# Performance work log

Hardware: AMD Instinct MI355X
Metric: run time of the kernel (lower is better)

Reference implementation:

```python
import jax, jax.numpy as jnp
import numpy as np

B1, B2, D = 8192, 12288, 128


def setup_inputs() -> dict:
    key = jax.random.key(0)
    k1, k2 = jax.random.split(key)
    desc1 = jax.random.normal(k1, (B1, D), dtype=jnp.float32)
    desc2 = jax.random.normal(k2, (B2, D), dtype=jnp.float32)
    return {"desc1": desc1, "desc2": desc2}


def reference(desc1, desc2):
    # Pairwise L2 distance (torch.cdist, p=2) via the expanded form to avoid
    sq1 = jnp.sum(desc1 * desc1, axis=1, keepdims=True)          # (B1, 1)
    sq2 = jnp.sum(desc2 * desc2, axis=1)                          # (B2,)
    cost = jnp.sqrt(jnp.maximum(sq1 + sq2 - 2.0 * (desc1 @ desc2.T), 0.0))  # (B1, B2)

    b1, b2 = cost.shape
    ms = min(b1, b2)

    match_dists = jnp.min(cost, axis=1)    # (B1,) row minima
    idxs_in_2 = jnp.argmin(cost, axis=1)   # (B1,)
    match_dists2 = jnp.min(cost, axis=0)   # (B2,) col minima
    idxs_in_1 = jnp.argmin(cost, axis=0)   # (B2,)

    minsize_idxs = jnp.arange(ms)
    if b1 <= b2:  # static shape comparison -> Python if is fine
        mutual_nns = minsize_idxs == idxs_in_1[idxs_in_2][:ms]
        dists = match_dists[:ms]
        matches_idxs = jnp.stack([minsize_idxs, idxs_in_2[:ms]], axis=1)
    else:
        mutual_nns = minsize_idxs == idxs_in_2[idxs_in_1][:ms]
        dists = match_dists2[:ms]
        matches_idxs = jnp.stack([idxs_in_1[:ms], minsize_idxs], axis=1)

    # jit-compatible fixed-size output: non-mutual rows are masked with
    # dist=+inf and idx=-1 instead of boolean-compressed as in torch.
    match_dists_out = jnp.where(mutual_nns, dists, jnp.inf).reshape(-1, 1)  # (ms, 1)
    matches_idxs_out = jnp.where(mutual_nns[:, None], matches_idxs, -1)      # (ms, 2)
    return match_dists_out, matches_idxs_out, mutual_nns
```

## Files before the change

### kernel.cpp

```cpp
#include <hip/hip_runtime.h>
#include <math.h>

#define NB1 8192
#define NB2 12288
#define DD  128

typedef unsigned long long u64;
typedef unsigned short ushort_t;
typedef __attribute__((ext_vector_type(8))) short short8;
typedef __attribute__((ext_vector_type(4))) float f32x4;

__device__ __forceinline__ float bigf() { return __uint_as_float(0x7F7F0000u); }

__device__ __forceinline__ unsigned orderbits(float v) {
    unsigned b = __float_as_uint(v);
    return b ^ ((unsigned)((int)b >> 31) | 0x80000000u);
}
__device__ __forceinline__ float unorderbits(unsigned k) {
    unsigned b = (k & 0x80000000u) ? (k ^ 0x80000000u) : ~k;
    return __uint_as_float(b);
}
__device__ __forceinline__ u64 packkey(float v, unsigned idx) {
    return ((u64)orderbits(v) << 32) | idx;
}
__device__ __forceinline__ u64 umin64(u64 a, u64 b) { return a < b ? a : b; }

__device__ __forceinline__ ushort_t bf_rn(float x) {
    unsigned u = __float_as_uint(x);
    return (ushort_t)((u + 0x7FFFu + ((u >> 16) & 1u)) >> 16);
}
__device__ __forceinline__ float bf_up(ushort_t h) {
    return __uint_as_float(((unsigned)h) << 16);
}
__device__ __forceinline__ int fswz(int r) { return (r + (r >> 2)) & 3; }

__global__ __launch_bounds__(256) void prep_kernel(
    const float* __restrict__ d1, const float* __restrict__ d2,
    float* __restrict__ sq1, float* __restrict__ sq2,
    u64* __restrict__ rowmin, u64* __restrict__ colmin) {
    int t = blockIdx.x * 256 + threadIdx.x;
    if (t < NB1) {
        rowmin[t] = ~0ull;
        const float4* p = (const float4*)(d1 + (size_t)t * DD);
        float s = 0.f;
        #pragma unroll
        for (int c = 0; c < DD / 4; ++c) {
            float4 v = p[c];
            s = fmaf(v.x, v.x, s); s = fmaf(v.y, v.y, s);
            s = fmaf(v.z, v.z, s); s = fmaf(v.w, v.w, s);
        }
        sq1[t] = s;
    }
    if (t < NB2) {
        colmin[t] = ~0ull;
        const float4* p = (const float4*)(d2 + (size_t)t * DD);
        float s = 0.f;
        #pragma unroll
        for (int c = 0; c < DD / 4; ++c) {
            float4 v = p[c];
            s = fmaf(v.x, v.x, s); s = fmaf(v.y, v.y, s);
            s = fmaf(v.z, v.z, s); s = fmaf(v.w, v.w, s);
        }
        sq2[t] = s;
    }
}

__global__ __launch_bounds__(256) void split_frag_kernel(
    const float* __restrict__ d1, const float* __restrict__ d2,
    ushort_t* __restrict__ Af, ushort_t* __restrict__ Bf) {
    int t = blockIdx.x * 256 + threadIdx.x;
    int lane = t & 63;
    int task = t >> 6;
    bool isA = task < 2048;
    int lt = isA ? task : task - 2048;
    int rb = lt >> 2;
    int kc = lt & 3;
    int row = rb * 16 + (lane & 15);
    int kst = kc * 32 + (lane >> 4) * 8;
    const float* src = (isA ? d1 : d2) + (size_t)row * DD + kst;
    size_t pstride = (size_t)(isA ? NB1 : NB2) * DD;
    ushort_t* dst = (isA ? Af : Bf) + ((size_t)lt * 512 + lane * 8);

    short8 H, M, L;
    #pragma unroll
    for (int e = 0; e < 8; ++e) {
        float x = src[e];
        ushort_t h = bf_rn(x); float r1 = x - bf_up(h);
        ushort_t m = bf_rn(r1); float r2 = r1 - bf_up(m);
        H[e] = (short)h; M[e] = (short)m; L[e] = (short)bf_rn(r2);
    }
    *(short8*)(dst)                = H;
    *(short8*)(dst + pstride)      = M;
    *(short8*)(dst + 2 * pstride)  = L;
}

__global__ __launch_bounds__(256) void mfma_tile3_kernel(
    const ushort_t* __restrict__ Af, const ushort_t* __restrict__ Bf,
    const float* __restrict__ sq1, const float* __restrict__ sq2,
    u64* __restrict__ rowmin, u64* __restrict__ colmin)
{
    const int bid  = blockIdx.x;
    const int xcd  = bid & 7;
    const int t_   = bid >> 3;
    const int kch  = t_ >> 6;
    const int wdn  = t_ & 63;
    const int cj   = wdn & 7;
    const int ci   = wdn >> 3;
    const int j0b  = (kch * 8 + cj) * 128;
    const int i0b  = (xcd * 8 + ci) * 128;

    const int tid  = threadIdx.x;
    const int lane = tid & 63;
    const int wid  = tid >> 6;
    const int wr   = wid >> 1;
    const int wc   = wid & 1;
    const int lrow = lane & 15;
    const int lg   = lane >> 4;

    const ushort_t* abase = Af + ((size_t)((i0b >> 4) + wr * 4) * 2048) + lane * 8;
    const ushort_t* bbase = Bf + ((size_t)((j0b >> 4) + wc * 4) * 2048) + lane * 8;
    const size_t apl = (size_t)512 * 2048;
    const size_t bpl = (size_t)768 * 2048;

    f32x4 acc[4][4];
    #pragma unroll
    for (int mi = 0; mi < 4; ++mi)
        #pragma unroll
        for (int ni = 0; ni < 4; ++ni)
            acc[mi][ni] = (f32x4){0.f, 0.f, 0.f, 0.f};

    #pragma unroll 1
    for (int kc = 0; kc < 4; ++kc) {
        const int ko = kc * 512;
        short8 bfr[3][4];
        #pragma unroll
        for (int c = 0; c < 3; ++c)
            #pragma unroll
            for (int ni = 0; ni < 4; ++ni)
                bfr[c][ni] = *(const short8*)(bbase + c * bpl + ni * 2048 + ko);
        short8 a0[3], a1[3];
        #pragma unroll
        for (int c = 0; c < 3; ++c)
            a0[c] = *(const short8*)(abase + c * apl + ko);
        #pragma unroll
        for (int mi = 0; mi < 4; ++mi) {
            if (mi < 3) {
                #pragma unroll
                for (int c = 0; c < 3; ++c)
                    a1[c] = *(const short8*)(abase + c * apl + (mi + 1) * 2048 + ko);
            }
            #pragma unroll
            for (int ni = 0; ni < 4; ++ni) {
                f32x4 a = acc[mi][ni];
                a = __builtin_amdgcn_mfma_f32_16x16x32_bf16(a0[0], bfr[0][ni], a, 0, 0, 0);
                a = __builtin_amdgcn_mfma_f32_16x16x32_bf16(a0[0], bfr[1][ni], a, 0, 0, 0);
                a = __builtin_amdgcn_mfma_f32_16x16x32_bf16(a0[1], bfr[0][ni], a, 0, 0, 0);
                a = __builtin_amdgcn_mfma_f32_16x16x32_bf16(a0[0], bfr[2][ni], a, 0, 0, 0);
                a = __builtin_amdgcn_mfma_f32_16x16x32_bf16(a0[1], bfr[1][ni], a, 0, 0, 0);
                a = __builtin_amdgcn_mfma_f32_16x16x32_bf16(a0[2], bfr[0][ni], a, 0, 0, 0);
                acc[mi][ni] = a;
            }
            #pragma unroll
            for (int c = 0; c < 3; ++c) a0[c] = a1[c];
        }
    }

    float q2v[4];
    #pragma unroll
    for (int ni = 0; ni < 4; ++ni)
        q2v[ni] = sq2[j0b + wc * 64 + ni * 16 + lrow];
    float4 q1v[4];
    #pragma unroll
    for (int mi = 0; mi < 4; ++mi)
        q1v[mi] = *(const float4*)(sq1 + i0b + wr * 64 + mi * 16 + 4 * lg);

    #pragma unroll
    for (int mi = 0; mi < 4; ++mi)
        #pragma unroll
        for (int r = 0; r < 4; ++r) {
            u64 best = ~0ull;
            #pragma unroll
            for (int ni = 0; ni < 4; ++ni) {
                float kr = fmaf(-2.f, acc[mi][ni][r], q2v[ni]);
                best = umin64(best, packkey(kr, (unsigned)(j0b + wc * 64 + ni * 16 + lrow)));
            }
            #pragma unroll
            for (int mask = 8; mask; mask >>= 1)
                best = umin64(best, __shfl_xor(best, mask));
            if (lrow == 0)
                atomicMin(&rowmin[i0b + wr * 64 + mi * 16 + 4 * lg + r], best);
        }

    #pragma unroll
    for (int ni = 0; ni < 4; ++ni) {
        u64 best = ~0ull;
        #pragma unroll
        for (int mi = 0; mi < 4; ++mi) {
            const float* q1p = (const float*)&q1v[mi];
            #pragma unroll
            for (int r = 0; r < 4; ++r) {
                float kc_ = fmaf(-2.f, acc[mi][ni][r], q1p[r]);
                best = umin64(best, packkey(kc_, (unsigned)(i0b + wr * 64 + mi * 16 + 4 * lg + r)));
            }
        }
        best = umin64(best, __shfl_xor(best, 16));
        best = umin64(best, __shfl_xor(best, 32));
        if (lane < 16)
            atomicMin(&colmin[j0b + wc * 64 + ni * 16 + lrow], best);
    }
}

__global__ __launch_bounds__(256) void mfma_tile_kernel(
    const float* __restrict__ d1, const float* __restrict__ d2,
    const float* __restrict__ sq1, const float* __restrict__ sq2,
    u64* __restrict__ rowmin, u64* __restrict__ colmin)
{
    __shared__ __align__(16) short lds[6 * 4096];
    const int tid = threadIdx.x;
    const int i0b = blockIdx.y * 128;
    const int j0b = blockIdx.x * 128;
    const int srow  = tid >> 1;
    const int shalf = tid & 1;
    const int sfr   = fswz(srow);
    const int sg0   = ((2 * shalf) ^ sfr) * 8;
    const int sg1   = ((2 * shalf + 1) ^ sfr) * 8;
    const float* gA = d1 + (size_t)(i0b + srow) * DD + shalf * 16;
    const float* gB = d2 + (size_t)(j0b + srow) * DD + shalf * 16;
    short* wA = lds + srow * 32;
    short* wB = lds + 3 * 4096 + srow * 32;
    const int lane = tid & 63;
    const int wid  = tid >> 6;
    const int wr   = wid >> 1;
    const int wc   = wid & 1;
    const int lrow = lane & 15;
    const int lg   = lane >> 4;
    const int gx   = (lg ^ fswz(lrow)) * 8;
    const int aoff = (wr * 64 + lrow) * 32 + gx;
    const int boff = 3 * 4096 + (wc * 64 + lrow) * 32 + gx;

    f32x4 acc[4][4];
    #pragma unroll
    for (int mi = 0; mi < 4; ++mi)
        #pragma unroll
        for (int ni = 0; ni < 4; ++ni)
            acc[mi][ni] = (f32x4){0.f, 0.f, 0.f, 0.f};

    for (int kc = 0; kc < 4; ++kc) {
        {
            const float* sp = gA + kc * 32;
            short8 H0, M0, L0, H1, M1, L1;
            #pragma unroll
            for (int e = 0; e < 8; ++e) {
                float x = sp[e];
                ushort_t h = bf_rn(x); float r1 = x - bf_up(h);
                ushort_t m = bf_rn(r1); float r2 = r1 - bf_up(m);
                H0[e] = (short)h; M0[e] = (short)m; L0[e] = (short)bf_rn(r2);
            }
            #pragma unroll
            for (int e = 0; e < 8; ++e) {
                float x = sp[8 + e];
                ushort_t h = bf_rn(x); float r1 = x - bf_up(h);
                ushort_t m = bf_rn(r1); float r2 = r1 - bf_up(m);
                H1[e] = (short)h; M1[e] = (short)m; L1[e] = (short)bf_rn(r2);
            }
            *(short8*)(wA + sg0)        = H0;
            *(short8*)(wA + sg1)        = H1;
            *(short8*)(wA + 4096 + sg0) = M0;
            *(short8*)(wA + 4096 + sg1) = M1;
            *(short8*)(wA + 8192 + sg0) = L0;
            *(short8*)(wA + 8192 + sg1) = L1;
        }
        {
            const float* sp = gB + kc * 32;
            short8 H0, M0, L0, H1, M1, L1;
            #pragma unroll
            for (int e = 0; e < 8; ++e) {
                float x = sp[e];
                ushort_t h = bf_rn(x); float r1 = x - bf_up(h);
                ushort_t m = bf_rn(r1); float r2 = r1 - bf_up(m);
                H0[e] = (short)h; M0[e] = (short)m; L0[e] = (short)bf_rn(r2);
            }
            #pragma unroll
            for (int e = 0; e < 8; ++e) {
                float x = sp[8 + e];
                ushort_t h = bf_rn(x); float r1 = x - bf_up(h);
                ushort_t m = bf_rn(r1); float r2 = r1 - bf_up(m);
                H1[e] = (short)h; M1[e] = (short)m; L1[e] = (short)bf_rn(r2);
            }
            *(short8*)(wB + sg0)        = H0;
            *(short8*)(wB + sg1)        = H1;
            *(short8*)(wB + 4096 + sg0) = M0;
            *(short8*)(wB + 4096 + sg1) = M1;
            *(short8*)(wB + 8192 + sg0) = L0;
            *(short8*)(wB + 8192 + sg1) = L1;
        }
        __syncthreads();
        short8 af[3][4], bfr[3][4];
        #pragma unroll
        for (int c = 0; c < 3; ++c)
            #pragma unroll
            for (int t = 0; t < 4; ++t) {
                af[c][t]  = *(const short8*)(lds + c * 4096 + aoff + t * 512);
                bfr[c][t] = *(const short8*)(lds + c * 4096 + boff + t * 512);
            }
        #pragma unroll
        for (int mi = 0; mi < 4; ++mi)
            #pragma unroll
            for (int ni = 0; ni < 4; ++ni) {
                f32x4 a = acc[mi][ni];
                a = __builtin_amdgcn_mfma_f32_16x16x32_bf16(af[0][mi], bfr[0][ni], a, 0, 0, 0);
                a = __builtin_amdgcn_mfma_f32_16x16x32_bf16(af[0][mi], bfr[1][ni], a, 0, 0, 0);
                a = __builtin_amdgcn_mfma_f32_16x16x32_bf16(af[1][mi], bfr[0][ni], a, 0, 0, 0);
                a = __builtin_amdgcn_mfma_f32_16x16x32_bf16(af[0][mi], bfr[2][ni], a, 0, 0, 0);
                a = __builtin_amdgcn_mfma_f32_16x16x32_bf16(af[1][mi], bfr[1][ni], a, 0, 0, 0);
                a = __builtin_amdgcn_mfma_f32_16x16x32_bf16(af[2][mi], bfr[0][ni], a, 0, 0, 0);
                acc[mi][ni] = a;
            }
        __syncthreads();
    }

    float q2v[4];
    #pragma unroll
    for (int ni = 0; ni < 4; ++ni)
        q2v[ni] = sq2[j0b + wc * 64 + ni * 16 + lrow];
    float4 q1v[4];
    #pragma unroll
    for (int mi = 0; mi < 4; ++mi)
        q1v[mi] = *(const float4*)(sq1 + i0b + wr * 64 + mi * 16 + 4 * lg);

    #pragma unroll
    for (int mi = 0; mi < 4; ++mi)
        #pragma unroll
        for (int r = 0; r < 4; ++r) {
            u64 best = ~0ull;
            #pragma unroll
            for (int ni = 0; ni < 4; ++ni) {
                float kr = fmaf(-2.f, acc[mi][ni][r], q2v[ni]);
                best = umin64(best, packkey(kr, (unsigned)(j0b + wc * 64 + ni * 16 + lrow)));
            }
            #pragma unroll
            for (int mask = 8; mask; mask >>= 1)
                best = umin64(best, __shfl_xor(best, mask));
            if (lrow == 0)
                atomicMin(&rowmin[i0b + wr * 64 + mi * 16 + 4 * lg + r], best);
        }
    #pragma unroll
    for (int ni = 0; ni < 4; ++ni) {
        u64 best = ~0ull;
        #pragma unroll
        for (int mi = 0; mi < 4; ++mi) {
            const float* q1p = (const float*)&q1v[mi];
            #pragma unroll
            for (int r = 0; r < 4; ++r) {
                float kc_ = fmaf(-2.f, acc[mi][ni][r], q1p[r]);
                best = umin64(best, packkey(kc_, (unsigned)(i0b + wr * 64 + mi * 16 + 4 * lg + r)));
            }
        }
        best = umin64(best, __shfl_xor(best, 16));
        best = umin64(best, __shfl_xor(best, 32));
        if (lane < 16)
            atomicMin(&colmin[j0b + wc * 64 + ni * 16 + lrow], best);
    }
}

__global__ __launch_bounds__(256) void final_kernel(
    const float* __restrict__ sq1,
    const u64* __restrict__ rowmin, const u64* __restrict__ colmin,
    float* __restrict__ out) {
    int i = blockIdx.x * 256 + threadIdx.x;
    if (i >= NB1) return;
    u64 rm = rowmin[i];
    unsigned ju = (unsigned)(rm & 0xFFFFFFFFu);
    float kr = unorderbits((unsigned)(rm >> 32));
    float dist = sqrtf(fmaxf(sq1[i] + kr, 0.f));
    dist = fminf(dist, bigf());
    bool valid = (ju < (unsigned)NB2);
    int j = valid ? (int)ju : 0;
    u64 cm = colmin[j];
    int i2 = (int)(cm & 0xFFFFFFFFu);
    bool mut = valid && (i2 == i);
    out[i] = mut ? dist : bigf();
    out[NB1 + 2 * i]     = mut ? (float)i : -1.f;
    out[NB1 + 2 * i + 1] = mut ? (float)j : -1.f;
    out[NB1 + 2 * NB1 + i] = mut ? 1.f : 0.f;
}

extern "C" void kernel_launch(void* const* d_in, const int* in_sizes, int n_in,
                              void* d_out, int out_size, void* d_ws, size_t ws_size,
                              hipStream_t stream) {
    const float* d1 = (const float*)d_in[0];
    const float* d2 = (const float*)d_in[1];
    float* out = (float*)d_out;

    char* ws = (char*)d_ws;
    float* sq1    = (float*)(ws);
    float* sq2    = (float*)(ws + 32768);
    u64*   rowmin = (u64*)(ws + 81920);
    u64*   colmin = (u64*)(ws + 147456);
    ushort_t* Af = (ushort_t*)(ws + 245760);
    ushort_t* Bf = (ushort_t*)(ws + 245760 + 6291456);
    const size_t need = 245760 + 6291456 + 9437184;

    hipLaunchKernelGGL(prep_kernel, dim3((NB2 + 255) / 256), dim3(256), 0, stream,
                       d1, d2, sq1, sq2, rowmin, colmin);
    if (ws_size >= need) {
        hipLaunchKernelGGL(split_frag_kernel, dim3(1280), dim3(256), 0, stream,
                           d1, d2, Af, Bf);
        hipLaunchKernelGGL(mfma_tile3_kernel, dim3((NB2 / 128) * (NB1 / 128)), dim3(256), 0, stream,
                           Af, Bf, sq1, sq2, rowmin, colmin);
    } else {
        hipLaunchKernelGGL(mfma_tile_kernel, dim3(NB2 / 128, NB1 / 128), dim3(256), 0, stream,
                           d1, d2, sq1, sq2, rowmin, colmin);
    }
    hipLaunchKernelGGL(final_kernel, dim3((NB1 + 255) / 256), dim3(256), 0, stream,
                       sq1, rowmin, colmin, out);
}
```

Baseline: 192.8 us.

## Interleave bf16 split planes per fragment and double-buffer B loads across k-chunks

The split kernel now stores the high, mid and low bf16 planes next to each other for each fragment, instead of in three separate plane arrays far apart. The GEMM kernel reads them with small contiguous offsets. The k-chunk loop is fully unrolled, with B fragments double-buffered and the next chunk's A fragment prefetched, so global loads overlap the MFMA work. This is meant to hide load latency and improve locality, at the cost of more live registers, which may reduce occupancy or cause spills.

After: 195.2 us. About the same (+1.3%).

```diff
diff --git a/kernel.cpp b/kernel.cpp
--- a/kernel.cpp
+++ b/kernel.cpp
@@ -33,6 +33,7 @@
     return __uint_as_float(((unsigned)h) << 16);
 }
 __device__ __forceinline__ int fswz(int r) { return (r + (r >> 2)) & 3; }
+__device__ __forceinline__ short8 ld8(const ushort_t* p) { return *(const short8*)p; }
 
 __global__ __launch_bounds__(256) void prep_kernel(
     const float* __restrict__ d1, const float* __restrict__ d2,
@@ -78,8 +79,7 @@
     int row = rb * 16 + (lane & 15);
     int kst = kc * 32 + (lane >> 4) * 8;
     const float* src = (isA ? d1 : d2) + (size_t)row * DD + kst;
-    size_t pstride = (size_t)(isA ? NB1 : NB2) * DD;
-    ushort_t* dst = (isA ? Af : Bf) + ((size_t)lt * 512 + lane * 8);
+    ushort_t* dst = (isA ? Af : Bf) + ((size_t)lt * 1536 + lane * 8);
 
     short8 H, M, L;
     #pragma unroll
@@ -89,9 +89,9 @@
         ushort_t m = bf_rn(r1); float r2 = r1 - bf_up(m);
         H[e] = (short)h; M[e] = (short)m; L[e] = (short)bf_rn(r2);
     }
-    *(short8*)(dst)                = H;
-    *(short8*)(dst + pstride)      = M;
-    *(short8*)(dst + 2 * pstride)  = L;
+    *(short8*)(dst)        = H;
+    *(short8*)(dst + 512)  = M;
+    *(short8*)(dst + 1024) = L;
 }
 
 __global__ __launch_bounds__(256) void mfma_tile3_kernel(
@@ -117,10 +117,8 @@
     const int lrow = lane & 15;
     const int lg   = lane >> 4;
 
-    const ushort_t* abase = Af + ((size_t)((i0b >> 4) + wr * 4) * 2048) + lane * 8;
-    const ushort_t* bbase = Bf + ((size_t)((j0b >> 4) + wc * 4) * 2048) + lane * 8;
-    const size_t apl = (size_t)512 * 2048;
-    const size_t bpl = (size_t)768 * 2048;
+    const ushort_t* abase = Af + ((size_t)((i0b >> 4) + wr * 4) * 6144) + lane * 8;
+    const ushort_t* bbase = Bf + ((size_t)((j0b >> 4) + wc * 4) * 6144) + lane * 8;
 
     f32x4 acc[4][4];
     #pragma unroll
@@ -129,35 +127,47 @@
         for (int ni = 0; ni < 4; ++ni)
             acc[mi][ni] = (f32x4){0.f, 0.f, 0.f, 0.f};
 
-    #pragma unroll 1
+    short8 bufA[3][4], bufB[3][4];
+    short8 a0[3], a1[3];
+    #pragma unroll
+    for (int c = 0; c < 3; ++c) {
+        #pragma unroll
+        for (int ni = 0; ni < 4; ++ni)
+            bufA[c][ni] = ld8(bbase + ni * 6144 + c * 512);
+        a0[c] = ld8(abase + c * 512);
+    }
+
+    #pragma unroll
     for (int kc = 0; kc < 4; ++kc) {
-        const int ko = kc * 512;
-        short8 bfr[3][4];
-        #pragma unroll
-        for (int c = 0; c < 3; ++c)
-            #pragma unroll
-            for (int ni = 0; ni < 4; ++ni)
-                bfr[c][ni] = *(const short8*)(bbase + c * bpl + ni * 2048 + ko);
-        short8 a0[3], a1[3];
-        #pragma unroll
-        for (int c = 0; c < 3; ++c)
-            a0[c] = *(const short8*)(abase + c * apl + ko);
+        short8 (&bc)[3][4] = (kc & 1) ? bufB : bufA;
+        short8 (&bn)[3][4] = (kc & 1) ? bufA : bufB;
+        if (kc < 3) {
+            #pragma unroll
+            for (int c = 0; c < 3; ++c)
+                #pragma unroll
+                for (int ni = 0; ni < 4; ++ni)
+                    bn[c][ni] = ld8(bbase + ni * 6144 + (kc + 1) * 1536 + c * 512);
+        }
         #pragma unroll
         for (int mi = 0; mi < 4; ++mi) {
             if (mi < 3) {
                 #pragma unroll
                 for (int c = 0; c < 3; ++c)
-                    a1[c] = *(const short8*)(abase + c * apl + (mi + 1) * 2048 + ko);
+                    a1[c] = ld8(abase + (mi + 1) * 6144 + kc * 1536 + c * 512);
+            } else if (kc < 3) {
+                #pragma unroll
+                for (int c = 0; c < 3; ++c)
+                    a1[c] = ld8(abase + (kc + 1) * 1536 + c * 512);
             }
             #pragma unroll
             for (int ni = 0; ni < 4; ++ni) {
                 f32x4 a = acc[mi][ni];
-                a = __builtin_amdgcn_mfma_f32_16x16x32_bf16(a0[0], bfr[0][ni], a, 0, 0, 0);
-                a = __builtin_amdgcn_mfma_f32_16x16x32_bf16(a0[0], bfr[1][ni], a, 0, 0, 0);
-                a = __builtin_amdgcn_mfma_f32_16x16x32_bf16(a0[1], bfr[0][ni], a, 0, 0, 0);
-                a = __builtin_amdgcn_mfma_f32_16x16x32_bf16(a0[0], bfr[2][ni], a, 0, 0, 0);
-                a = __builtin_amdgcn_mfma_f32_16x16x32_bf16(a0[1], bfr[1][ni], a, 0, 0, 0);
-                a = __builtin_amdgcn_mfma_f32_16x16x32_bf16(a0[2], bfr[0][ni], a, 0, 0, 0);
+                a = __builtin_amdgcn_mfma_f32_16x16x32_bf16(a0[0], bc[0][ni], a, 0, 0, 0);
+                a = __builtin_amdgcn_mfma_f32_16x16x32_bf16(a0[0], bc[1][ni], a, 0, 0, 0);
+                a = __builtin_amdgcn_mfma_f32_16x16x32_bf16(a0[1], bc[0][ni], a, 0, 0, 0);
+                a = __builtin_amdgcn_mfma_f32_16x16x32_bf16(a0[0], bc[2][ni], a, 0, 0, 0);
+                a = __builtin_amdgcn_mfma_f32_16x16x32_bf16(a0[1], bc[1][ni], a, 0, 0, 0);
+                a = __builtin_amdgcn_mfma_f32_16x16x32_bf16(a0[2], bc[0][ni], a, 0, 0, 0);
                 acc[mi][ni] = a;
             }
             #pragma unroll
```

## Replace 3-way bf16 split GEMM with 2-way scaled fp16 split

Applied to the files above, without the earlier changes.

Switches the emulated-fp32 distance GEMM from a three-piece bf16 decomposition (six MFMAs per tile step) to a two-piece fp16 decomposition with the residual scaled by 2048 (three MFMAs per step, kept in two accumulators and recombined at the end). This halves matrix-core work and cuts fragment memory traffic and workspace from three planes to two. The risk is lower accuracy: fp16 range and precision on the residual could change argmin ties or near-equal distances compared with the fp32 reference.

Result: slower. 272.2 us (+41.2%).

```diff
diff --git a/kernel.cpp b/kernel.cpp
--- a/kernel.cpp
+++ b/kernel.cpp
@@ -8,6 +8,7 @@
 typedef unsigned long long u64;
 typedef unsigned short ushort_t;
 typedef __attribute__((ext_vector_type(8))) short short8;
+typedef __attribute__((ext_vector_type(8))) _Float16 half8;
 typedef __attribute__((ext_vector_type(4))) float f32x4;
 
 __device__ __forceinline__ float bigf() { return __uint_as_float(0x7F7F0000u); }
@@ -33,6 +34,7 @@
     return __uint_as_float(((unsigned)h) << 16);
 }
 __device__ __forceinline__ int fswz(int r) { return (r + (r >> 2)) & 3; }
+__device__ __forceinline__ half8 ld8h(const _Float16* p) { return *(const half8*)p; }
 
 __global__ __launch_bounds__(256) void prep_kernel(
     const float* __restrict__ d1, const float* __restrict__ d2,
@@ -65,9 +67,9 @@
     }
 }
 
-__global__ __launch_bounds__(256) void split_frag_kernel(
+__global__ __launch_bounds__(256) void split_frag16_kernel(
     const float* __restrict__ d1, const float* __restrict__ d2,
-    ushort_t* __restrict__ Af, ushort_t* __restrict__ Bf) {
+    _Float16* __restrict__ Af, _Float16* __restrict__ Bf) {
     int t = blockIdx.x * 256 + threadIdx.x;
     int lane = t & 63;
     int task = t >> 6;
@@ -78,24 +80,24 @@
     int row = rb * 16 + (lane & 15);
     int kst = kc * 32 + (lane >> 4) * 8;
     const float* src = (isA ? d1 : d2) + (size_t)row * DD + kst;
-    size_t pstride = (size_t)(isA ? NB1 : NB2) * DD;
-    ushort_t* dst = (isA ? Af : Bf) + ((size_t)lt * 512 + lane * 8);
-
-    short8 H, M, L;
+    const size_t plane = (size_t)(isA ? NB1 : NB2) * DD;
+    _Float16* dst = (isA ? Af : Bf) + ((size_t)lt * 512 + lane * 8);
+
+    half8 H, M;
     #pragma unroll
     for (int e = 0; e < 8; ++e) {
         float x = src[e];
-        ushort_t h = bf_rn(x); float r1 = x - bf_up(h);
-        ushort_t m = bf_rn(r1); float r2 = r1 - bf_up(m);
-        H[e] = (short)h; M[e] = (short)m; L[e] = (short)bf_rn(r2);
-    }
-    *(short8*)(dst)                = H;
-    *(short8*)(dst + pstride)      = M;
-    *(short8*)(dst + 2 * pstride)  = L;
-}
-
-__global__ __launch_bounds__(256) void mfma_tile3_kernel(
-    const ushort_t* __restrict__ Af, const ushort_t* __restrict__ Bf,
+        _Float16 h = (_Float16)x;
+        float m = x - (float)h;
+        H[e] = h;
+        M[e] = (_Float16)(m * 2048.0f);
+    }
+    *(half8*)(dst)         = H;
+    *(half8*)(dst + plane) = M;
+}
+
+__global__ __launch_bounds__(256) void mfma_tile6_kernel(
+    const _Float16* __restrict__ Af, const _Float16* __restrict__ Bf,
     const float* __restrict__ sq1, const float* __restrict__ sq2,
     u64* __restrict__ rowmin, u64* __restrict__ colmin)
 {
@@ -104,10 +106,8 @@
     const int t_   = bid >> 3;
     const int kch  = t_ >> 6;
     const int wdn  = t_ & 63;
-    const int cj   = wdn & 7;
-    const int ci   = wdn >> 3;
-    const int j0b  = (kch * 8 + cj) * 128;
-    const int i0b  = (xcd * 8 + ci) * 128;
+    const int j0b  = (kch * 8 + (wdn & 7)) * 128;
+    const int i0b  = (xcd * 8 + (wdn >> 3)) * 128;
 
     const int tid  = threadIdx.x;
     const int lane = tid & 63;
@@ -117,54 +117,51 @@
     const int lrow = lane & 15;
     const int lg   = lane >> 4;
 
-    const ushort_t* abase = Af + ((size_t)((i0b >> 4) + wr * 4) * 2048) + lane * 8;
-    const ushort_t* bbase = Bf + ((size_t)((j0b >> 4) + wc * 4) * 2048) + lane * 8;
-    const size_t apl = (size_t)512 * 2048;
-    const size_t bpl = (size_t)768 * 2048;
-
-    f32x4 acc[4][4];
-    #pragma unroll
-    for (int mi = 0; mi < 4; ++mi)
-        #pragma unroll
-        for (int ni = 0; ni < 4; ++ni)
-            acc[mi][ni] = (f32x4){0.f, 0.f, 0.f, 0.f};
+    const _Float16* abase = Af + ((size_t)((i0b >> 4) + wr * 4) * 2048) + lane * 8;
+    const _Float16* bbase = Bf + ((size_t)((j0b >> 4) + wc * 4) * 2048) + lane * 8;
+    const size_t paf = (size_t)NB1 * DD;
+    const size_t pbf = (size_t)NB2 * DD;
+
+    f32x4 acc0[4][4], acc1[4][4];
+    #pragma unroll
+    for (int mi = 0; mi < 4; ++mi)
+        #pragma unroll
+        for (int ni = 0; ni < 4; ++ni) {
+            acc0[mi][ni] = (f32x4){0.f, 0.f, 0.f, 0.f};
+            acc1[mi][ni] = (f32x4){0.f, 0.f, 0.f, 0.f};
+        }
 
     #pragma unroll 1
     for (int kc = 0; kc < 4; ++kc) {
         const int ko = kc * 512;
-        short8 bfr[3][4];
-        #pragma unroll
-        for (int c = 0; c < 3; ++c)
-            #pragma unroll
-            for (int ni = 0; ni < 4; ++ni)
-                bfr[c][ni] = *(const short8*)(bbase + c * bpl + ni * 2048 + ko);
-        short8 a0[3], a1[3];
-        #pragma unroll
-        for (int c = 0; c < 3; ++c)
-            a0[c] = *(const short8*)(abase + c * apl + ko);
+        half8 bh[4], bm[4];
+        #pragma unroll
+        for (int ni = 0; ni < 4; ++ni) {
+            bh[ni] = ld8h(bbase + ni * 2048 + ko);
+            bm[ni] = ld8h(bbase + pbf + ni * 2048 + ko);
+        }
+        half8 ah0, am0, ah1, am1;
+        ah0 = ld8h(abase + ko);
+        am0 = ld8h(abase + paf + ko);
         #pragma unroll
         for (int mi = 0; mi < 4; ++mi) {
             if (mi < 3) {
-                #pragma unroll
-                for (int c = 0; c < 3; ++c)
-                    a1[c] = *(const short8*)(abase + c * apl + (mi + 1) * 2048 + ko);
+                ah1 = ld8h(abase + (mi + 1) * 2048 + ko);
+                am1 = ld8h(abase + paf + (mi + 1) * 2048 + ko);
             }
             #pragma unroll
             for (int ni = 0; ni < 4; ++ni) {
-                f32x4 a = acc[mi][ni];
-                a = __builtin_amdgcn_mfma_f32_16x16x32_bf16(a0[0], bfr[0][ni], a, 0, 0, 0);
-                a = __builtin_amdgcn_mfma_f32_16x16x32_bf16(a0[0], bfr[1][ni], a, 0, 0, 0);
-                a = __builtin_amdgcn_mfma_f32_16x16x32_bf16(a0[1], bfr[0][ni], a, 0, 0, 0);
-                a = __builtin_amdgcn_mfma_f32_16x16x32_bf16(a0[0], bfr[2][ni], a, 0, 0, 0);
-                a = __builtin_amdgcn_mfma_f32_16x16x32_bf16(a0[1], bfr[1][ni], a, 0, 0, 0);
-                a = __builtin_amdgcn_mfma_f32_16x16x32_bf16(a0[2], bfr[0][ni], a, 0, 0, 0);
-                acc[mi][ni] = a;
-            }
-            #pragma unroll
-            for (int c = 0; c < 3; ++c) a0[c] = a1[c];
-        }
-    }
-
+                acc0[mi][ni] = __builtin_amdgcn_mfma_f32_16x16x32_f16(ah0, bh[ni], acc0[mi][ni], 0, 0, 0);
+                f32x4 t = acc1[mi][ni];
+                t = __builtin_amdgcn_mfma_f32_16x16x32_f16(ah0, bm[ni], t, 0, 0, 0);
+                t = __builtin_amdgcn_mfma_f32_16x16x32_f16(am0, bh[ni], t, 0, 0, 0);
+                acc1[mi][ni] = t;
+            }
+            ah0 = ah1; am0 = am1;
+        }
+    }
+
+    const float SC = 0.00048828125f;
     float q2v[4];
     #pragma unroll
     for (int ni = 0; ni < 4; ++ni)
@@ -181,7 +178,8 @@
             u64 best = ~0ull;
             #pragma unroll
             for (int ni = 0; ni < 4; ++ni) {
-                float kr = fmaf(-2.f, acc[mi][ni][r], q2v[ni]);
+                float d = fmaf(acc1[mi][ni][r], SC, acc0[mi][ni][r]);
+                float kr = fmaf(-2.f, d, q2v[ni]);
                 best = umin64(best, packkey(kr, (unsigned)(j0b + wc * 64 + ni * 16 + lrow)));
             }
             #pragma unroll
@@ -199,7 +197,8 @@
             const float* q1p = (const float*)&q1v[mi];
             #pragma unroll
             for (int r = 0; r < 4; ++r) {
-                float kc_ = fmaf(-2.f, acc[mi][ni][r], q1p[r]);
+                float d = fmaf(acc1[mi][ni][r], SC, acc0[mi][ni][r]);
+                float kc_ = fmaf(-2.f, d, q1p[r]);
                 best = umin64(best, packkey(kc_, (unsigned)(i0b + wr * 64 + mi * 16 + 4 * lg + r)));
             }
         }
@@ -397,16 +396,16 @@
     float* sq2    = (float*)(ws + 32768);
     u64*   rowmin = (u64*)(ws + 81920);
     u64*   colmin = (u64*)(ws + 147456);
-    ushort_t* Af = (ushort_t*)(ws + 245760);
-    ushort_t* Bf = (ushort_t*)(ws + 245760 + 6291456);
-    const size_t need = 245760 + 6291456 + 9437184;
+    _Float16* Af = (_Float16*)(ws + 245760);
+    _Float16* Bf = (_Float16*)(ws + 245760 + 4194304);
+    const size_t need = 245760 + 4194304 + 6291456;
 
     hipLaunchKernelGGL(prep_kernel, dim3((NB2 + 255) / 256), dim3(256), 0, stream,
                        d1, d2, sq1, sq2, rowmin, colmin);
     if (ws_size >= need) {
-        hipLaunchKernelGGL(split_frag_kernel, dim3(1280), dim3(256), 0, stream,
+        hipLaunchKernelGGL(split_frag16_kernel, dim3(1280), dim3(256), 0, stream,
                            d1, d2, Af, Bf);
-        hipLaunchKernelGGL(mfma_tile3_kernel, dim3((NB2 / 128) * (NB1 / 128)), dim3(256), 0, stream,
+        hipLaunchKernelGGL(mfma_tile6_kernel, dim3(6144), dim3(256), 0, stream,
                            Af, Bf, sq1, sq2, rowmin, colmin);
     } else {
         hipLaunchKernelGGL(mfma_tile_kernel, dim3(NB2 / 128, NB1 / 128), dim3(256), 0, stream,
```
